# Optimization experiments

Hardware: AMD Instinct MI355X
Metric: run time of the kernel (lower is better)

## Reference

```python
import jax, jax.numpy as jnp
import numpy as np

K_HOPS = 10  # truncation order of the heat-kernel Taylor series


def setup_inputs() -> dict:
    key = jax.random.key(0)
    k1, k2, k3 = jax.random.split(key, 3)
    N, E, D_IN, D_OUT = 50000, 625000, 128, 128
    x = jax.random.normal(k1, (N, D_IN), dtype=jnp.float32)
    edge_index = jax.random.randint(k2, (2, E), 0, N, dtype=jnp.int64)
    t = jnp.asarray(5.0, dtype=jnp.float32)  # learnable diffusion time
    lim = 1.0 / np.sqrt(D_IN)
    W = jax.random.uniform(k3, (D_OUT, D_IN), dtype=jnp.float32, minval=-lim, maxval=lim)
    b = jnp.zeros((D_OUT,), dtype=jnp.float32)
    return {"x": x, "edge_index": edge_index, "t": t, "W": W, "b": b}


def reference(x, edge_index, t, W, b):
    N = x.shape[0]
    loop = jnp.arange(N, dtype=edge_index.dtype)
    src = jnp.concatenate([edge_index[0], loop])  # gcn_norm adds self-loops
    dst = jnp.concatenate([edge_index[1], loop])
    # symmetric normalization: norm_e = deg(dst)^-1/2 * deg(src)^-1/2
    deg = jnp.zeros((N,), dtype=x.dtype).at[dst].add(1.0)
    dinv = jnp.where(deg > 0, jax.lax.rsqrt(deg), 0.0)
    norm = dinv[src] * dinv[dst]  # [E+N]

    def prop(h):  # one hop of A_hat @ h via gather-scale-scatter
        msg = h[src] * norm[:, None]          # [E+N, D]
        return jax.ops.segment_sum(msg, dst, num_segments=N)

    # heat kernel: e^{-t} * sum_k t^k/k! * A_hat^k x
    coeff = jnp.exp(-t)
    out = coeff * x
    h = x
    for k in range(1, K_HOPS + 1):
        h = prop(h)
        coeff = coeff * t / k
        out = out + coeff * h
    return out @ W.T + b
```

## Files before the change

kernel.cpp:

```cpp
#include <hip/hip_runtime.h>
#include <math.h>

typedef float f4 __attribute__((ext_vector_type(4)));
typedef float f8 __attribute__((ext_vector_type(8)));
typedef _Float16 h8 __attribute__((ext_vector_type(8)));


__global__ void k_count(const int* __restrict__ dst, int* __restrict__ cnt, int E) {
  int e = blockIdx.x * blockDim.x + threadIdx.x;
  if (e < E) atomicAdd(&cnt[dst[e]], 1);
}

__global__ void k_scan_partial(const int* __restrict__ cnt, int* __restrict__ rowptr,
                               int* __restrict__ bsums, float* __restrict__ dinv, int N) {
  __shared__ int s[1024];
  int tid = threadIdx.x;
  int idx = blockIdx.x * 1024 + tid;
  int v = (idx < N) ? cnt[idx] : 0;
  if (idx < N) dinv[idx] = rsqrtf((float)(v + 1));
  int vp = (v + 3) & ~3;
  s[tid] = vp;
  __syncthreads();
  for (int off = 1; off < 1024; off <<= 1) {
    int add = (tid >= off) ? s[tid - off] : 0;
    __syncthreads();
    s[tid] += add;
    __syncthreads();
  }
  if (idx <= N) rowptr[idx] = s[tid] - vp;
  if (tid == 1023) bsums[blockIdx.x] = s[1023];
}

__global__ void k_scan_sums(int* __restrict__ bsums, int nb) {
  __shared__ int s[1024];
  int tid = threadIdx.x;
  int v = (tid < nb) ? bsums[tid] : 0;
  s[tid] = v;
  __syncthreads();
  for (int off = 1; off < 1024; off <<= 1) {
    int add = (tid >= off) ? s[tid - off] : 0;
    __syncthreads();
    s[tid] += add;
    __syncthreads();
  }
  if (tid < nb) bsums[tid] = s[tid] - v;
}

__global__ void k_add_offsets(int* __restrict__ rowptr, int* __restrict__ cursor,
                              const int* __restrict__ bsums, int N) {
  int idx = blockIdx.x * 1024 + threadIdx.x;
  if (idx <= N) {
    int v = rowptr[idx] + bsums[blockIdx.x];
    rowptr[idx] = v;
    if (idx < N) cursor[idx] = v;
  }
}

__global__ void k_scatter(const int* __restrict__ src, const int* __restrict__ dst,
                          const float* __restrict__ dinv, int* __restrict__ cursor,
                          int2* __restrict__ colw, int E) {
  int e = blockIdx.x * blockDim.x + threadIdx.x;
  if (e < E) {
    int s = src[e];
    int d = dst[e];
    int slot = atomicAdd(&cursor[d], 1);
    colw[slot] = make_int2(s, __float_as_int(dinv[s] * dinv[d]));
  }
}

__global__ void k_tohalf(const float* __restrict__ x, _Float16* __restrict__ xh, int total8) {
  int i = blockIdx.x * blockDim.x + threadIdx.x;
  if (i < total8) {
    f4 a = ((const f4*)x)[i * 2], b = ((const f4*)x)[i * 2 + 1];
    f8 v = {a.x, a.y, a.z, a.w, b.x, b.y, b.z, b.w};
    ((h8*)xh)[i] = __builtin_convertvector(v, h8);
  }
}

__global__ __launch_bounds__(256) void k_hop(
    const int* __restrict__ rowptr, const int2* __restrict__ colw,
    const float* __restrict__ dinv, const h8* __restrict__ xh,
    const h8* __restrict__ yin, h8* __restrict__ yout,
    const float* __restrict__ t_ptr, int j, int first, int N) {
  int wave = threadIdx.x >> 6;
  int lane = threadIdx.x & 63;
  int grp = lane >> 3;
  int r = (blockIdx.x * 4 + wave) * 4 + (grp >> 1);
  if (r >= N) return;
  int fl = (lane & 7) + (grp & 1) * 8;
  float t = t_ptr[0];
  float cj = expf(-t);
  for (int i = 1; i <= j; ++i) cj *= t / (float)i;
  float gs = first ? cj * t / (float)(j + 1) : 1.0f;

  auto G = [&](int idx) -> f8 {
    return __builtin_convertvector(yin[(size_t)idx * 16 + fl], f8);
  };

  f8 sA = {0,0,0,0,0,0,0,0}, sB = sA, sC = sA, sD = sA;
  int e = rowptr[r], end = rowptr[r + 1];
  for (; e < end; e += 4) {
    int4 p0 = *(const int4*)&colw[e];
    int4 p1 = *(const int4*)&colw[e + 2];
    sA += __int_as_float(p0.y) * G(p0.x);
    sB += __int_as_float(p0.w) * G(p0.z);
    sC += __int_as_float(p1.y) * G(p1.x);
    sD += __int_as_float(p1.w) * G(p1.z);
  }
  f8 s = (sA + sB) + (sC + sD);
  float di = dinv[r];
  s += (di * di) * G(r);
  f8 xr = __builtin_convertvector(xh[(size_t)r * 16 + fl], f8);
  s = gs * s + cj * xr;
  yout[(size_t)r * 16 + fl] = __builtin_convertvector(s, h8);
}

__global__ __launch_bounds__(256) void k_matmul(
    const h8* __restrict__ y16, const float* __restrict__ W,
    const float* __restrict__ bias, float* __restrict__ out, int N) {
  __shared__ h8 whiS[128 * 16];
  __shared__ h8 wloS[128 * 16];
  int tid = threadIdx.x;
  int rblk = blockIdx.x * 128;

#pragma unroll
  for (int it = 0; it < 8; ++it) {
    int idx = it * 256 + tid;
    int n = idx >> 4, g = idx & 15;
    f4 a = *(const f4*)&W[(size_t)n * 128 + g * 8];
    f4 b = *(const f4*)&W[(size_t)n * 128 + g * 8 + 4];
    f8 w = {a.x, a.y, a.z, a.w, b.x, b.y, b.z, b.w};
    h8 hi = __builtin_convertvector(w, h8);
    f8 hir = __builtin_convertvector(hi, f8);
    h8 lo = __builtin_convertvector(w - hir, h8);
    int slot = n * 16 + (g ^ (n & 7));
    whiS[slot] = hi;
    wloS[slot] = lo;
  }
  __syncthreads();

  int wave = tid >> 6, lane = tid & 63;
  int q = lane >> 4, fl = lane & 15;
  int rbase = rblk + wave * 32;

  f4 acc[2][8];
#pragma unroll
  for (int rt = 0; rt < 2; ++rt)
#pragma unroll
    for (int nt = 0; nt < 8; ++nt) acc[rt][nt] = (f4){0.f, 0.f, 0.f, 0.f};

#pragma unroll
  for (int s = 0; s < 4; ++s) {
    h8 aA, aB;
    {
      int r0 = rbase + fl;       if (r0 >= N) r0 = N - 1;
      int r1 = rbase + 16 + fl;  if (r1 >= N) r1 = N - 1;
      aA = y16[(size_t)r0 * 16 + s * 4 + q];
      aB = y16[(size_t)r1 * 16 + s * 4 + q];
    }
#pragma unroll
    for (int nt = 0; nt < 8; ++nt) {
      int n = nt * 16 + fl;
      int slot = n * 16 + ((s * 4 + q) ^ (n & 7));
      h8 bh = whiS[slot];
      h8 bl = wloS[slot];
      acc[0][nt] = __builtin_amdgcn_mfma_f32_16x16x32_f16(aA, bh, acc[0][nt], 0, 0, 0);
      acc[0][nt] = __builtin_amdgcn_mfma_f32_16x16x32_f16(aA, bl, acc[0][nt], 0, 0, 0);
      acc[1][nt] = __builtin_amdgcn_mfma_f32_16x16x32_f16(aB, bh, acc[1][nt], 0, 0, 0);
      acc[1][nt] = __builtin_amdgcn_mfma_f32_16x16x32_f16(aB, bl, acc[1][nt], 0, 0, 0);
    }
  }

#pragma unroll
  for (int rt = 0; rt < 2; ++rt) {
#pragma unroll
    for (int nt = 0; nt < 8; ++nt) {
      float bv = bias[nt * 16 + fl];
#pragma unroll
      for (int reg = 0; reg < 4; ++reg) {
        int r = rbase + rt * 16 + q * 4 + reg;
        if (r < N) out[(size_t)r * 128 + nt * 16 + fl] = acc[rt][nt][reg] + bv;
      }
    }
  }
}


extern "C" void kernel_launch(void* const* d_in, const int* in_sizes, int n_in,
                              void* d_out, int out_size, void* d_ws, size_t ws_size,
                              hipStream_t stream) {
  const float* x = (const float*)d_in[0];
  const int* ei = (const int*)d_in[1];
  const float* t = (const float*)d_in[2];
  const float* W = (const float*)d_in[3];
  const float* b = (const float*)d_in[4];
  int N = in_sizes[0] / 128;
  int E = in_sizes[1] / 2;
  const int* srcp = ei;
  const int* dstp = ei + E;
  float* out = (float*)d_out;

  char* ws = (char*)d_ws;
  size_t off = 0;
  auto alloc = [&](size_t bytes) -> void* {
    void* p = ws + off;
    off += (bytes + 255) & ~(size_t)255;
    return p;
  };
  h8*    yh0    = (h8*)alloc((size_t)N * 128 * 2);
  h8*    yh1    = (h8*)alloc((size_t)N * 128 * 2);
  h8*    xh     = (h8*)alloc((size_t)N * 128 * 2);
  int*   cnt    = (int*)alloc((size_t)N * 4);
  float* dinv   = (float*)alloc((size_t)N * 4);
  int*   rowptr = (int*)alloc((size_t)(N + 1) * 4);
  int*   cursor = (int*)alloc((size_t)N * 4);
  int*   bsums  = (int*)alloc(4096);
  size_t colw_bytes = ((size_t)E + 4 * (size_t)N) * 8;
  int2*  colw   = (int2*)alloc(colw_bytes);
  (void)ws_size;

  int nb_scan = (N + 1 + 1023) / 1024;

  hipMemsetAsync(cnt, 0, (size_t)N * 4, stream);
  hipMemsetAsync(colw, 0, colw_bytes, stream);
  k_count<<<(E + 255) / 256, 256, 0, stream>>>(dstp, cnt, E);
  k_scan_partial<<<nb_scan, 1024, 0, stream>>>(cnt, rowptr, bsums, dinv, N);
  k_scan_sums<<<1, 1024, 0, stream>>>(bsums, nb_scan);
  k_add_offsets<<<nb_scan, 1024, 0, stream>>>(rowptr, cursor, bsums, N);
  k_scatter<<<(E + 255) / 256, 256, 0, stream>>>(srcp, dstp, dinv, cursor, colw, E);
  k_tohalf<<<(N * 16 + 255) / 256, 256, 0, stream>>>(x, (_Float16*)xh, N * 16);

  int nblk = (N + 15) / 16;
  const h8* yin = xh;
  h8* bufs[2] = {yh0, yh1};
  for (int m = 0; m < 10; ++m) {
    h8* yout = bufs[m & 1];
    k_hop<<<nblk, 256, 0, stream>>>(rowptr, colw, dinv, xh, yin, yout,
                                    t, 9 - m, (m == 0) ? 1 : 0, N);
    yin = yout;
  }

  k_matmul<<<(N + 127) / 128, 256, 0, stream>>>(yin, W, b, out, N);
}
```

Baseline: 444.1 us.

## Split each row's edges across two lane groups, software-pipeline edge loads, nontemporal hints

Each destination row in the hop kernel is now handled by 32 lanes instead of 16: two lane halves take alternating 4-edge chunks and combine their partial sums with a cross-lane shuffle. The edge-pair loads are software-pipelined one iteration ahead, and nontemporal load/store hints are added for the colw, x, y and output streams. The aim is more memory-level parallelism per row and shorter per-wave loops for the gather-bound SpMM. In exchange it uses twice as many blocks, adds shuffle overhead, and leaves lanes idle on short rows.

```diff
diff --git a/kernel.cpp b/kernel.cpp
--- a/kernel.cpp
+++ b/kernel.cpp
@@ -4,6 +4,7 @@
 typedef float f4 __attribute__((ext_vector_type(4)));
 typedef float f8 __attribute__((ext_vector_type(8)));
 typedef _Float16 h8 __attribute__((ext_vector_type(8)));
+typedef int i4 __attribute__((ext_vector_type(4)));
 
 
 __global__ void k_count(const int* __restrict__ dst, int* __restrict__ cnt, int E) {
@@ -85,9 +86,10 @@
   int wave = threadIdx.x >> 6;
   int lane = threadIdx.x & 63;
   int grp = lane >> 3;
-  int r = (blockIdx.x * 4 + wave) * 4 + (grp >> 1);
+  int part = grp & 1;
+  int r = (blockIdx.x * 4 + wave) * 2 + (grp >> 2);
   if (r >= N) return;
-  int fl = (lane & 7) + (grp & 1) * 8;
+  int fl = (lane & 7) + ((grp >> 1) & 1) * 8;
   float t = t_ptr[0];
   float cj = expf(-t);
   for (int i = 1; i <= j; ++i) cj *= t / (float)i;
@@ -97,22 +99,47 @@
     return __builtin_convertvector(yin[(size_t)idx * 16 + fl], f8);
   };
 
-  f8 sA = {0,0,0,0,0,0,0,0}, sB = sA, sC = sA, sD = sA;
-  int e = rowptr[r], end = rowptr[r + 1];
-  for (; e < end; e += 4) {
-    int4 p0 = *(const int4*)&colw[e];
-    int4 p1 = *(const int4*)&colw[e + 2];
+  float di = 0.f;
+  f8 selfv = {0, 0, 0, 0, 0, 0, 0, 0};
+  f8 xr = selfv;
+  if (!part) {
+    di = dinv[r];
+    selfv = G(r);
+    xr = __builtin_convertvector(__builtin_nontemporal_load(&xh[(size_t)r * 16 + fl]), f8);
+  }
+
+  f8 sA = {0, 0, 0, 0, 0, 0, 0, 0}, sB = sA, sC = sA, sD = sA;
+  const i4* cw = (const i4*)colw;
+  int e = rowptr[r] + (part << 2);
+  int end = rowptr[r + 1];
+  if (e < end) {
+    i4 p0 = __builtin_nontemporal_load(&cw[e >> 1]);
+    i4 p1 = __builtin_nontemporal_load(&cw[(e >> 1) + 1]);
+    for (e += 8; e < end; e += 8) {
+      i4 q0 = __builtin_nontemporal_load(&cw[e >> 1]);
+      i4 q1 = __builtin_nontemporal_load(&cw[(e >> 1) + 1]);
+      sA += __int_as_float(p0.y) * G(p0.x);
+      sB += __int_as_float(p0.w) * G(p0.z);
+      sC += __int_as_float(p1.y) * G(p1.x);
+      sD += __int_as_float(p1.w) * G(p1.z);
+      p0 = q0;
+      p1 = q1;
+    }
     sA += __int_as_float(p0.y) * G(p0.x);
     sB += __int_as_float(p0.w) * G(p0.z);
     sC += __int_as_float(p1.y) * G(p1.x);
     sD += __int_as_float(p1.w) * G(p1.z);
   }
   f8 s = (sA + sB) + (sC + sD);
-  float di = dinv[r];
-  s += (di * di) * G(r);
-  f8 xr = __builtin_convertvector(xh[(size_t)r * 16 + fl], f8);
-  s = gs * s + cj * xr;
-  yout[(size_t)r * 16 + fl] = __builtin_convertvector(s, h8);
+#pragma unroll
+  for (int k = 0; k < 8; ++k) s[k] += __shfl_xor(s[k], 8, 64);
+
+  if (!part) {
+    s += (di * di) * selfv;
+    s = gs * s + cj * xr;
+    __builtin_nontemporal_store(__builtin_convertvector(s, h8),
+                                &yout[(size_t)r * 16 + fl]);
+  }
 }
 
 __global__ __launch_bounds__(256) void k_matmul(
@@ -155,8 +182,8 @@
     {
       int r0 = rbase + fl;       if (r0 >= N) r0 = N - 1;
       int r1 = rbase + 16 + fl;  if (r1 >= N) r1 = N - 1;
-      aA = y16[(size_t)r0 * 16 + s * 4 + q];
-      aB = y16[(size_t)r1 * 16 + s * 4 + q];
+      aA = __builtin_nontemporal_load(&y16[(size_t)r0 * 16 + s * 4 + q]);
+      aB = __builtin_nontemporal_load(&y16[(size_t)r1 * 16 + s * 4 + q]);
     }
 #pragma unroll
     for (int nt = 0; nt < 8; ++nt) {
@@ -179,7 +206,10 @@
 #pragma unroll
       for (int reg = 0; reg < 4; ++reg) {
         int r = rbase + rt * 16 + q * 4 + reg;
-        if (r < N) out[(size_t)r * 128 + nt * 16 + fl] = acc[rt][nt][reg] + bv;
+        if (r < N) {
+          float v = acc[rt][nt][reg] + bv;
+          __builtin_nontemporal_store(v, &out[(size_t)r * 128 + nt * 16 + fl]);
+        }
       }
     }
   }
@@ -230,7 +260,7 @@
   k_scatter<<<(E + 255) / 256, 256, 0, stream>>>(srcp, dstp, dinv, cursor, colw, E);
   k_tohalf<<<(N * 16 + 255) / 256, 256, 0, stream>>>(x, (_Float16*)xh, N * 16);
 
-  int nblk = (N + 15) / 16;
+  int nblk = (N + 7) / 8;
   const h8* yin = xh;
   h8* bufs[2] = {yh0, yh1};
   for (int m = 0; m < 10; ++m) {
```

After: 474.6 us. 1.07x slower.

## Rescale features by D^-1/2 to drop per-edge weights from CSR

Applied to the files above, without the earlier changes.

The diffusion is rewritten in the rescaled variable z = D^-1/2 y, so each hop becomes an unweighted neighbour sum scaled once per row by dinv^2, and the final sqrt(deg) factor is applied in the matmul epilogue. The CSR now holds only column indices (4 bytes instead of 8 per edge), and padding slots point to a zeroed dummy row N in place of zero weights. The gather loop is software-pipelined over 8 indices at a time. This halves the index traffic and removes the per-edge multiply, but adds a pad-fill kernel, a dummy row in each buffer, and some extra fp16 rounding from the rescaling.

```diff
diff --git a/kernel.cpp b/kernel.cpp
--- a/kernel.cpp
+++ b/kernel.cpp
@@ -4,6 +4,7 @@
 typedef float f4 __attribute__((ext_vector_type(4)));
 typedef float f8 __attribute__((ext_vector_type(8)));
 typedef _Float16 h8 __attribute__((ext_vector_type(8)));
+typedef int i4 __attribute__((ext_vector_type(4)));
 
 
 __global__ void k_count(const int* __restrict__ dst, int* __restrict__ cnt, int E) {
@@ -12,12 +13,16 @@
 }
 
 __global__ void k_scan_partial(const int* __restrict__ cnt, int* __restrict__ rowptr,
-                               int* __restrict__ bsums, float* __restrict__ dinv, int N) {
+                               int* __restrict__ bsums, float* __restrict__ dinv,
+                               float* __restrict__ rdinv, int N) {
   __shared__ int s[1024];
   int tid = threadIdx.x;
   int idx = blockIdx.x * 1024 + tid;
   int v = (idx < N) ? cnt[idx] : 0;
-  if (idx < N) dinv[idx] = rsqrtf((float)(v + 1));
+  if (idx < N) {
+    dinv[idx] = rsqrtf((float)(v + 1));
+    rdinv[idx] = sqrtf((float)(v + 1));
+  }
   int vp = (v + 3) & ~3;
   s[tid] = vp;
   __syncthreads();
@@ -57,30 +62,46 @@
 }
 
 __global__ void k_scatter(const int* __restrict__ src, const int* __restrict__ dst,
-                          const float* __restrict__ dinv, int* __restrict__ cursor,
-                          int2* __restrict__ colw, int E) {
+                          int* __restrict__ cursor, int* __restrict__ col, int E) {
   int e = blockIdx.x * blockDim.x + threadIdx.x;
   if (e < E) {
-    int s = src[e];
     int d = dst[e];
     int slot = atomicAdd(&cursor[d], 1);
-    colw[slot] = make_int2(s, __float_as_int(dinv[s] * dinv[d]));
-  }
-}
-
-__global__ void k_tohalf(const float* __restrict__ x, _Float16* __restrict__ xh, int total8) {
+    col[slot] = src[e];
+  }
+}
+
+__global__ void k_padfill(const int* __restrict__ rowptr, const int* __restrict__ cursor,
+                          int* __restrict__ col, int N) {
+  int r = blockIdx.x * blockDim.x + threadIdx.x;
+  if (r < N) {
+    int e = cursor[r], end = rowptr[r + 1];
+    for (; e < end; ++e) col[e] = N;
+  }
+}
+
+__global__ void k_tohalf(const float* __restrict__ x, _Float16* __restrict__ xz,
+                         const float* __restrict__ dinv, _Float16* __restrict__ z0,
+                         _Float16* __restrict__ z1, int total8) {
   int i = blockIdx.x * blockDim.x + threadIdx.x;
   if (i < total8) {
+    float d = dinv[i >> 4];
     f4 a = ((const f4*)x)[i * 2], b = ((const f4*)x)[i * 2 + 1];
     f8 v = {a.x, a.y, a.z, a.w, b.x, b.y, b.z, b.w};
-    ((h8*)xh)[i] = __builtin_convertvector(v, h8);
+    ((h8*)xz)[i] = __builtin_convertvector(d * v, h8);
+  } else if (i < total8 + 48) {
+    int k = i - total8;
+    h8 zero = {0, 0, 0, 0, 0, 0, 0, 0};
+    if (k < 16) ((h8*)xz)[total8 + k] = zero;
+    else if (k < 32) ((h8*)z0)[total8 + (k - 16)] = zero;
+    else ((h8*)z1)[total8 + (k - 32)] = zero;
   }
 }
 
 __global__ __launch_bounds__(256) void k_hop(
-    const int* __restrict__ rowptr, const int2* __restrict__ colw,
-    const float* __restrict__ dinv, const h8* __restrict__ xh,
-    const h8* __restrict__ yin, h8* __restrict__ yout,
+    const int* __restrict__ rowptr, const int* __restrict__ col,
+    const float* __restrict__ dinv, const h8* __restrict__ xz,
+    const h8* __restrict__ zin, h8* __restrict__ zout,
     const float* __restrict__ t_ptr, int j, int first, int N) {
   int wave = threadIdx.x >> 6;
   int lane = threadIdx.x & 63;
@@ -94,30 +115,65 @@
   float gs = first ? cj * t / (float)(j + 1) : 1.0f;
 
   auto G = [&](int idx) -> f8 {
-    return __builtin_convertvector(yin[(size_t)idx * 16 + fl], f8);
+    return __builtin_convertvector(zin[(size_t)idx * 16 + fl], f8);
   };
 
-  f8 sA = {0,0,0,0,0,0,0,0}, sB = sA, sC = sA, sD = sA;
+  f8 sA = {0, 0, 0, 0, 0, 0, 0, 0}, sB = sA, sC = sA, sD = sA;
   int e = rowptr[r], end = rowptr[r + 1];
-  for (; e < end; e += 4) {
-    int4 p0 = *(const int4*)&colw[e];
-    int4 p1 = *(const int4*)&colw[e + 2];
-    sA += __int_as_float(p0.y) * G(p0.x);
-    sB += __int_as_float(p0.w) * G(p0.z);
-    sC += __int_as_float(p1.y) * G(p1.x);
-    sD += __int_as_float(p1.w) * G(p1.z);
-  }
+  int cnt = end - e;
+  const i4* q = (const i4*)&col[e];
+  int it8 = cnt >> 3;
+  int tail4 = cnt & 7;
+
+  i4 p0 = {0, 0, 0, 0}, p1 = p0;
+  if (it8) {
+    p0 = q[0]; p1 = q[1];
+    q += 2;
+  }
+  for (int i = 1; i < it8; ++i) {
+    i4 n0 = q[0], n1 = q[1];
+    q += 2;
+    sA += G(p0.x);
+    sB += G(p0.y);
+    sC += G(p0.z);
+    sD += G(p0.w);
+    sA += G(p1.x);
+    sB += G(p1.y);
+    sC += G(p1.z);
+    sD += G(p1.w);
+    p0 = n0; p1 = n1;
+  }
+  if (it8) {
+    sA += G(p0.x);
+    sB += G(p0.y);
+    sC += G(p0.z);
+    sD += G(p0.w);
+    sA += G(p1.x);
+    sB += G(p1.y);
+    sC += G(p1.z);
+    sD += G(p1.w);
+  }
+  if (tail4) {
+    i4 a0 = q[0];
+    sA += G(a0.x);
+    sB += G(a0.y);
+    sC += G(a0.z);
+    sD += G(a0.w);
+  }
+
   f8 s = (sA + sB) + (sC + sD);
+  s += G(r);
   float di = dinv[r];
-  s += (di * di) * G(r);
-  f8 xr = __builtin_convertvector(xh[(size_t)r * 16 + fl], f8);
-  s = gs * s + cj * xr;
-  yout[(size_t)r * 16 + fl] = __builtin_convertvector(s, h8);
+  float sc = gs * di * di;
+  f8 xr = __builtin_convertvector(xz[(size_t)r * 16 + fl], f8);
+  s = sc * s + cj * xr;
+  zout[(size_t)r * 16 + fl] = __builtin_convertvector(s, h8);
 }
 
 __global__ __launch_bounds__(256) void k_matmul(
-    const h8* __restrict__ y16, const float* __restrict__ W,
-    const float* __restrict__ bias, float* __restrict__ out, int N) {
+    const h8* __restrict__ z16, const float* __restrict__ W,
+    const float* __restrict__ bias, const float* __restrict__ rdinv,
+    float* __restrict__ out, int N) {
   __shared__ h8 whiS[128 * 16];
   __shared__ h8 wloS[128 * 16];
   int tid = threadIdx.x;
@@ -155,8 +211,8 @@
     {
       int r0 = rbase + fl;       if (r0 >= N) r0 = N - 1;
       int r1 = rbase + 16 + fl;  if (r1 >= N) r1 = N - 1;
-      aA = y16[(size_t)r0 * 16 + s * 4 + q];
-      aB = y16[(size_t)r1 * 16 + s * 4 + q];
+      aA = z16[(size_t)r0 * 16 + s * 4 + q];
+      aB = z16[(size_t)r1 * 16 + s * 4 + q];
     }
 #pragma unroll
     for (int nt = 0; nt < 8; ++nt) {
@@ -174,12 +230,15 @@
 #pragma unroll
   for (int rt = 0; rt < 2; ++rt) {
 #pragma unroll
-    for (int nt = 0; nt < 8; ++nt) {
-      float bv = bias[nt * 16 + fl];
-#pragma unroll
-      for (int reg = 0; reg < 4; ++reg) {
-        int r = rbase + rt * 16 + q * 4 + reg;
-        if (r < N) out[(size_t)r * 128 + nt * 16 + fl] = acc[rt][nt][reg] + bv;
+    for (int reg = 0; reg < 4; ++reg) {
+      int r = rbase + rt * 16 + q * 4 + reg;
+      if (r < N) {
+        float rd = rdinv[r];
+#pragma unroll
+        for (int nt = 0; nt < 8; ++nt) {
+          out[(size_t)r * 128 + nt * 16 + fl] =
+              acc[rt][nt][reg] * rd + bias[nt * 16 + fl];
+        }
       }
     }
   }
@@ -207,38 +266,41 @@
     off += (bytes + 255) & ~(size_t)255;
     return p;
   };
-  h8*    yh0    = (h8*)alloc((size_t)N * 128 * 2);
-  h8*    yh1    = (h8*)alloc((size_t)N * 128 * 2);
-  h8*    xh     = (h8*)alloc((size_t)N * 128 * 2);
+  h8*    zh0    = (h8*)alloc((size_t)(N + 1) * 128 * 2);
+  h8*    zh1    = (h8*)alloc((size_t)(N + 1) * 128 * 2);
+  h8*    xz     = (h8*)alloc((size_t)(N + 1) * 128 * 2);
   int*   cnt    = (int*)alloc((size_t)N * 4);
   float* dinv   = (float*)alloc((size_t)N * 4);
+  float* rdinv  = (float*)alloc((size_t)N * 4);
   int*   rowptr = (int*)alloc((size_t)(N + 1) * 4);
   int*   cursor = (int*)alloc((size_t)N * 4);
   int*   bsums  = (int*)alloc(4096);
-  size_t colw_bytes = ((size_t)E + 4 * (size_t)N) * 8;
-  int2*  colw   = (int2*)alloc(colw_bytes);
+  size_t col_bytes = ((size_t)E + 4 * (size_t)N) * 4;
+  int*   col    = (int*)alloc(col_bytes);
   (void)ws_size;
 
   int nb_scan = (N + 1 + 1023) / 1024;
 
   hipMemsetAsync(cnt, 0, (size_t)N * 4, stream);
-  hipMemsetAsync(colw, 0, colw_bytes, stream);
   k_count<<<(E + 255) / 256, 256, 0, stream>>>(dstp, cnt, E);
-  k_scan_partial<<<nb_scan, 1024, 0, stream>>>(cnt, rowptr, bsums, dinv, N);
+  k_scan_partial<<<nb_scan, 1024, 0, stream>>>(cnt, rowptr, bsums, dinv, rdinv, N);
   k_scan_sums<<<1, 1024, 0, stream>>>(bsums, nb_scan);
   k_add_offsets<<<nb_scan, 1024, 0, stream>>>(rowptr, cursor, bsums, N);
-  k_scatter<<<(E + 255) / 256, 256, 0, stream>>>(srcp, dstp, dinv, cursor, colw, E);
-  k_tohalf<<<(N * 16 + 255) / 256, 256, 0, stream>>>(x, (_Float16*)xh, N * 16);
+  k_scatter<<<(E + 255) / 256, 256, 0, stream>>>(srcp, dstp, cursor, col, E);
+  k_padfill<<<(N + 255) / 256, 256, 0, stream>>>(rowptr, cursor, col, N);
+  k_tohalf<<<(N * 16 + 48 + 255) / 256, 256, 0, stream>>>(x, (_Float16*)xz, dinv,
+                                                          (_Float16*)zh0, (_Float16*)zh1,
+                                                          N * 16);
 
   int nblk = (N + 15) / 16;
-  const h8* yin = xh;
-  h8* bufs[2] = {yh0, yh1};
+  const h8* zin = xz;
+  h8* bufs[2] = {zh0, zh1};
   for (int m = 0; m < 10; ++m) {
-    h8* yout = bufs[m & 1];
-    k_hop<<<nblk, 256, 0, stream>>>(rowptr, colw, dinv, xh, yin, yout,
+    h8* zout = bufs[m & 1];
+    k_hop<<<nblk, 256, 0, stream>>>(rowptr, col, dinv, xz, zin, zout,
                                     t, 9 - m, (m == 0) ? 1 : 0, N);
-    yin = yout;
-  }
-
-  k_matmul<<<(N + 127) / 128, 256, 0, stream>>>(yin, W, b, out, N);
-}
+    zin = zout;
+  }
+
+  k_matmul<<<(N + 127) / 128, 256, 0, stream>>>(zin, W, b, rdinv, out, N);
+}
```

After: 430.4 us, median of 2. -3.1%, faster.
